# Kernel optimization log

Hardware: AMD Instinct MI355X
Metric: run time of the kernel (lower is better)

## Reference

```python
import jax, jax.numpy as jnp
import numpy as np

NUM_GRAPHS = 4096   # number of systems in the batch
NUM_ATOMS = 262144  # total ragged atoms (~64 per graph)
MODEL_DIMS = 512
VOCAB = 100         # atomic-number vocabulary


def setup_inputs() -> dict:
    key = jax.random.key(0)
    ks = jax.random.split(key, 8)
    atomic_numbers = jax.random.randint(ks[0], (NUM_ATOMS,), 0, VOCAB)
    pos = jax.random.normal(ks[1], (NUM_ATOMS, 3), dtype=jnp.float32)
    batch = jnp.sort(jax.random.randint(ks[2], (NUM_ATOMS,), 0, NUM_GRAPHS))
    embed = jax.random.normal(ks[3], (VOCAB, MODEL_DIMS), dtype=jnp.float32) * 0.02
    w_pos = jax.random.normal(ks[4], (3, MODEL_DIMS), dtype=jnp.float32) * 0.02
    w1 = jax.random.normal(ks[5], (MODEL_DIMS, MODEL_DIMS), dtype=jnp.float32) / np.sqrt(MODEL_DIMS)
    b1 = jnp.zeros((MODEL_DIMS,), dtype=jnp.float32)
    w2 = jax.random.normal(ks[6], (MODEL_DIMS, 1), dtype=jnp.float32) / np.sqrt(MODEL_DIMS)
    b2 = jnp.zeros((1,), dtype=jnp.float32)
    return dict(atomic_numbers=atomic_numbers, pos=pos, batch=batch,
                embed=embed, w_pos=w_pos, w1=w1, b1=b1, w2=w2, b2=b2)


def reference(atomic_numbers, pos, batch, embed, w_pos, w1, b1, w2, b2):
    # atom_rr.prepare_inputs: per-atom feature = type embedding + linear position
    # encoding, reduced to a per-graph mean (segment mean replaces the original
    # Python loop over ragged graph slices).
    feats = embed[atomic_numbers] + pos @ w_pos                      # [N, D]
    summed = jax.ops.segment_sum(feats, batch, num_segments=NUM_GRAPHS)    # [G, D]
    counts = jax.ops.segment_sum(jnp.ones((NUM_ATOMS,), feats.dtype), batch,
                                 num_segments=NUM_GRAPHS)            # [G]
    reduced = summed / jnp.maximum(counts, 1.0)[:, None]             # [G, D]
    # net: Linear -> GELU -> Linear
    h = jax.nn.gelu(reduced @ w1 + b1)                               # [G, D]
    energy = h @ w2 + b2                                             # [G, 1]
    return energy
```

## Files before the change

kernel.cpp:

```cpp
#include <hip/hip_runtime.h>
#include <hip/hip_bf16.h>
#include <math.h>

#define NATOMS 262144
#define NGRAPH 4096
#define DIM    512
#define VOC    100
#define GPB    16
#define KC     8
#define KLEN   (DIM / KC)
#define ROWS   104
#define HROW   104


__device__ __forceinline__ float gelu_tanh(float x) {
    const float c = 0.7978845608028654f;
    float x3 = x * x * x;
    return 0.5f * x * (1.0f + tanhf(c * (x + 0.044715f * x3)));
}

__device__ __forceinline__ int lower_bound(const int* __restrict__ a, int n, int t) {
    int lo = 0, hi = n;
    while (lo < hi) {
        int mid = (lo + hi) >> 1;
        if (a[mid] < t) lo = mid + 1; else hi = mid;
    }
    return lo;
}

__global__ void k_fused(const int* __restrict__ an, const float* __restrict__ pos,
                        const int* __restrict__ batch,
                        const float* __restrict__ embed, const float* __restrict__ w_pos,
                        const float* __restrict__ w1,
                        float* __restrict__ Hf, float* __restrict__ partial, int n) {
    const int t = threadIdx.x;

    if (blockIdx.x < NGRAPH / GPB) {
        const int g0 = blockIdx.x * GPB;

        __shared__ int   lh[GPB][VOC];
        __shared__ float lps[GPB][3];
        __shared__ int   lcnt[GPB];
        __shared__ int   range[2];

        for (int idx = t; idx < GPB * VOC; idx += 256) ((int*)lh)[idx] = 0;
        if (t < GPB * 3) ((float*)lps)[t] = 0.0f;
        if (t < GPB)     lcnt[t] = 0;
        if (t == 0) range[0] = lower_bound(batch, n, g0);
        if (t == 1) range[1] = lower_bound(batch, n, g0 + GPB);
        __syncthreads();

        const int lo = range[0], hi = range[1];

        for (int base = lo; base < hi; base += 256) {
            int i = base + t;
            bool act = (i < hi);
            int ic = act ? i : (hi - 1);
            int g = batch[ic];
            int rel = g - g0;

            float px = 0.f, py = 0.f, pz = 0.f;
            if (act) {
                int v = an[i];
                px = pos[3 * i + 0];
                py = pos[3 * i + 1];
                pz = pos[3 * i + 2];
                atomicAdd(&lh[rel][v], 1);
            }

            int lane = t & 63;
            int gFirst = __shfl(g, 0);
            int gLast  = __shfl(g, 63);
            if (gFirst == gLast) {
                float sx = px, sy = py, sz = pz;
                int   sc = act ? 1 : 0;
                #pragma unroll
                for (int off = 32; off; off >>= 1) {
                    sx += __shfl_down(sx, off);
                    sy += __shfl_down(sy, off);
                    sz += __shfl_down(sz, off);
                    sc += __shfl_down(sc, off);
                }
                if (lane == 0 && sc > 0) {
                    atomicAdd(&lps[rel][0], sx);
                    atomicAdd(&lps[rel][1], sy);
                    atomicAdd(&lps[rel][2], sz);
                    atomicAdd(&lcnt[rel], sc);
                }
            } else if (act) {
                atomicAdd(&lps[rel][0], px);
                atomicAdd(&lps[rel][1], py);
                atomicAdd(&lps[rel][2], pz);
                atomicAdd(&lcnt[rel], 1);
            }
        }
        __syncthreads();

        for (int idx = t; idx < GPB * HROW; idx += 256) {
            int u = idx / HROW, c = idx - u * HROW;
            float inv = 1.0f / fmaxf((float)lcnt[u], 1.0f);
            float val = 0.0f;
            if (c < VOC)          val = (float)lh[u][c] * inv;
            else if (c < VOC + 3) val = lps[u][c - VOC] * inv;
            Hf[(size_t)(g0 + u) * HROW + c] = val;
        }
    } else {
        const int mb = blockIdx.x - NGRAPH / GPB;
        const int kc = mb & (KC - 1);
        const int rc = mb >> 3;
        const int rt = rc >> 1;
        const int cc = rc & 1;
        const int j  = cc * 256 + t;
        const int r0 = rt * 8;
        const int k0 = kc * KLEN;

        __shared__ float s[8][KLEN];
        for (int idx = t; idx < 8 * KLEN; idx += 256) {
            int rr = idx / KLEN, k = idx & (KLEN - 1);
            int r = r0 + rr;
            float val = 0.0f;
            if (r < VOC)          val = embed[r * DIM + k0 + k];
            else if (r < VOC + 3) val = w_pos[(r - VOC) * DIM + k0 + k];
            s[rr][k] = val;
        }
        __syncthreads();

        float acc[8];
        #pragma unroll
        for (int rr = 0; rr < 8; rr++) acc[rr] = 0.0f;

        #pragma unroll 8
        for (int k = 0; k < KLEN; k++) {
            float w = w1[(k0 + k) * DIM + j];
            #pragma unroll
            for (int rr = 0; rr < 8; rr++)
                acc[rr] = fmaf(s[rr][k], w, acc[rr]);
        }

        #pragma unroll
        for (int rr = 0; rr < 8; rr++)
            partial[((size_t)kc * ROWS + r0 + rr) * DIM + j] = acc[rr];
    }
}

__global__ void k_reduce(const float* __restrict__ partial, float* __restrict__ M1) {
    int idx = blockIdx.x * 256 + threadIdx.x;
    if (idx >= 103 * DIM) return;
    int r = idx / DIM, j = idx - r * DIM;
    float sum = 0.0f;
    #pragma unroll
    for (int kc = 0; kc < KC; kc++)
        sum += partial[((size_t)kc * ROWS + r) * DIM + j];
    M1[r * DIM + j] = sum;
}

__global__ void k_final(const float* __restrict__ Hf, const float* __restrict__ M1,
                        const float* __restrict__ b1, const float* __restrict__ w2,
                        const float* __restrict__ b2, float* __restrict__ out) {
    const int G0 = blockIdx.x * 16;
    const int j = threadIdx.x;

    __shared__ float hT[HROW][20];
    __shared__ float part[8][16];

    for (int idx = j; idx < 16 * HROW; idx += 512) {
        int u = idx / HROW;
        int v = idx - u * HROW;
        hT[v][u] = Hf[(size_t)(G0 + u) * HROW + v];
    }
    __syncthreads();

    float acc[16];
    #pragma unroll
    for (int u = 0; u < 16; u++) acc[u] = 0.0f;

    for (int v = 0; v < VOC + 3; v++) {
        float m = M1[v * DIM + j];
        const float4* hp = (const float4*)(&hT[v][0]);
        float4 h0 = hp[0], h1 = hp[1], h2 = hp[2], h3 = hp[3];
        acc[ 0] = fmaf(h0.x, m, acc[ 0]);
        acc[ 1] = fmaf(h0.y, m, acc[ 1]);
        acc[ 2] = fmaf(h0.z, m, acc[ 2]);
        acc[ 3] = fmaf(h0.w, m, acc[ 3]);
        acc[ 4] = fmaf(h1.x, m, acc[ 4]);
        acc[ 5] = fmaf(h1.y, m, acc[ 5]);
        acc[ 6] = fmaf(h1.z, m, acc[ 6]);
        acc[ 7] = fmaf(h1.w, m, acc[ 7]);
        acc[ 8] = fmaf(h2.x, m, acc[ 8]);
        acc[ 9] = fmaf(h2.y, m, acc[ 9]);
        acc[10] = fmaf(h2.z, m, acc[10]);
        acc[11] = fmaf(h2.w, m, acc[11]);
        acc[12] = fmaf(h3.x, m, acc[12]);
        acc[13] = fmaf(h3.y, m, acc[13]);
        acc[14] = fmaf(h3.z, m, acc[14]);
        acc[15] = fmaf(h3.w, m, acc[15]);
    }

    float bj = b1[j];
    float wj = w2[j];
    float contrib[16];
    #pragma unroll
    for (int u = 0; u < 16; u++) {
        float pre = acc[u] + bj;
        contrib[u] = gelu_tanh(pre) * wj;
    }

    int wave = j >> 6;
    int lane = j & 63;
    #pragma unroll
    for (int u = 0; u < 16; u++) {
        float s = contrib[u];
        #pragma unroll
        for (int off = 32; off; off >>= 1) s += __shfl_down(s, off);
        if (lane == 0) part[wave][u] = s;
    }
    __syncthreads();

    if (j < 16) {
        float e = 0.0f;
        #pragma unroll
        for (int w = 0; w < 8; w++) e += part[w][j];
        out[G0 + j] = e + b2[0];
    }
}

extern "C" void kernel_launch(void* const* d_in, const int* in_sizes, int n_in,
                              void* d_out, int out_size, void* d_ws, size_t ws_size,
                              hipStream_t stream) {
    const int*   an    = (const int*)d_in[0];
    const float* pos   = (const float*)d_in[1];
    const int*   batch = (const int*)d_in[2];
    const float* embed = (const float*)d_in[3];
    const float* w_pos = (const float*)d_in[4];
    const float* w1    = (const float*)d_in[5];
    const float* b1    = (const float*)d_in[6];
    const float* w2    = (const float*)d_in[7];
    const float* b2    = (const float*)d_in[8];
    float* out = (float*)d_out;

    const int n = in_sizes[0];

    char* ws = (char*)d_ws;
    const size_t HF_B = (size_t)NGRAPH * HROW * 4;
    const size_t M1_B = (size_t)103 * DIM * 4;
    float* Hf      = (float*)ws;
    float* M1      = (float*)(ws + HF_B);
    float* partial = (float*)(ws + HF_B + M1_B);

    const int AB = NGRAPH / GPB;
    const int MB = 13 * 2 * KC;
    k_fused<<<AB + MB, 256, 0, stream>>>(an, pos, batch, embed, w_pos, w1,
                                         Hf, partial, n);
    k_reduce<<<(103 * DIM + 255) / 256, 256, 0, stream>>>(partial, M1);

    k_final<<<NGRAPH / 16, 512, 0, stream>>>(Hf, M1, b1, w2, b2, out);
}
```

Baseline: 111.5 us.

## Fuse three kernels into one cooperative kernel with grid-wide syncs

Merges the histogram/matmul, partial-reduce, and final GELU-projection kernels into a single cooperative launch of 512 blocks, separated by grid.sync() barriers. The final stage is re-tiled so each block handles 8 graphs with 256 threads covering two output columns each. The aim is to remove the launch gaps between kernels. In exchange it pays for two grid-wide barriers, and it falls back to the old three-kernel path if the cooperative launch fails.

New measurement: 231.0 us. 2.07x slower.

```diff
diff --git a/kernel.cpp b/kernel.cpp
--- a/kernel.cpp
+++ b/kernel.cpp
@@ -1,6 +1,8 @@
 #include <hip/hip_runtime.h>
-#include <hip/hip_bf16.h>
+#include <hip/hip_cooperative_groups.h>
 #include <math.h>
+
+namespace cg = cooperative_groups;
 
 #define NATOMS 262144
 #define NGRAPH 4096
@@ -11,6 +13,11 @@
 #define KLEN   (DIM / KC)
 #define ROWS   104
 #define HROW   104
+#define NBLK   512
+#define NTHR   256
+#define AB     256
+#define MB     208
+#define G3     8
 
 
 __device__ __forceinline__ float gelu_tanh(float x) {
@@ -28,22 +35,29 @@
     return lo;
 }
 
-__global__ void k_fused(const int* __restrict__ an, const float* __restrict__ pos,
-                        const int* __restrict__ batch,
-                        const float* __restrict__ embed, const float* __restrict__ w_pos,
-                        const float* __restrict__ w1,
-                        float* __restrict__ Hf, float* __restrict__ partial, int n) {
+__global__ void k_all(const int* __restrict__ an, const float* __restrict__ pos,
+                      const int* __restrict__ batch,
+                      const float* __restrict__ embed, const float* __restrict__ w_pos,
+                      const float* __restrict__ w1, const float* __restrict__ b1,
+                      const float* __restrict__ w2, const float* __restrict__ b2,
+                      float* __restrict__ Hf, float* __restrict__ partial,
+                      float* __restrict__ M1, float* __restrict__ out, int n) {
+    cg::grid_group grid = cg::this_grid();
+    const int b = blockIdx.x;
     const int t = threadIdx.x;
 
-    if (blockIdx.x < NGRAPH / GPB) {
-        const int g0 = blockIdx.x * GPB;
-
-        __shared__ int   lh[GPB][VOC];
-        __shared__ float lps[GPB][3];
-        __shared__ int   lcnt[GPB];
-        __shared__ int   range[2];
-
-        for (int idx = t; idx < GPB * VOC; idx += 256) ((int*)lh)[idx] = 0;
+    __shared__ int   lh[GPB][VOC];
+    __shared__ float lps[GPB][3];
+    __shared__ int   lcnt[GPB];
+    __shared__ int   range[2];
+    __shared__ float smat[8][KLEN];
+    __shared__ __align__(16) float hT[ROWS][G3];
+    __shared__ float part[4][G3];
+
+    if (b < AB) {
+        const int g0 = b * GPB;
+
+        for (int idx = t; idx < GPB * VOC; idx += NTHR) ((int*)lh)[idx] = 0;
         if (t < GPB * 3) ((float*)lps)[t] = 0.0f;
         if (t < GPB)     lcnt[t] = 0;
         if (t == 0) range[0] = lower_bound(batch, n, g0);
@@ -52,7 +66,7 @@
 
         const int lo = range[0], hi = range[1];
 
-        for (int base = lo; base < hi; base += 256) {
+        for (int base = lo; base < hi; base += NTHR) {
             int i = base + t;
             bool act = (i < hi);
             int ic = act ? i : (hi - 1);
@@ -96,6 +110,173 @@
         }
         __syncthreads();
 
+        for (int idx = t; idx < GPB * HROW; idx += NTHR) {
+            int u = idx / HROW, c = idx - u * HROW;
+            float inv = 1.0f / fmaxf((float)lcnt[u], 1.0f);
+            float val = 0.0f;
+            if (c < VOC)          val = (float)lh[u][c] * inv;
+            else if (c < VOC + 3) val = lps[u][c - VOC] * inv;
+            Hf[(size_t)(g0 + u) * HROW + c] = val;
+        }
+    } else if (b < AB + MB) {
+        const int mb = b - AB;
+        const int kc = mb & (KC - 1);
+        const int rc = mb >> 3;
+        const int rt = rc >> 1;
+        const int cc = rc & 1;
+        const int j  = cc * 256 + t;
+        const int r0 = rt * 8;
+        const int k0 = kc * KLEN;
+
+        for (int idx = t; idx < 8 * KLEN; idx += NTHR) {
+            int rr = idx / KLEN, k = idx & (KLEN - 1);
+            int r = r0 + rr;
+            float val = 0.0f;
+            if (r < VOC)          val = embed[r * DIM + k0 + k];
+            else if (r < VOC + 3) val = w_pos[(r - VOC) * DIM + k0 + k];
+            smat[rr][k] = val;
+        }
+        __syncthreads();
+
+        float acc[8];
+        #pragma unroll
+        for (int rr = 0; rr < 8; rr++) acc[rr] = 0.0f;
+
+        #pragma unroll 8
+        for (int k = 0; k < KLEN; k++) {
+            float w = w1[(k0 + k) * DIM + j];
+            #pragma unroll
+            for (int rr = 0; rr < 8; rr++)
+                acc[rr] = fmaf(smat[rr][k], w, acc[rr]);
+        }
+
+        #pragma unroll
+        for (int rr = 0; rr < 8; rr++)
+            partial[((size_t)kc * ROWS + r0 + rr) * DIM + j] = acc[rr];
+    }
+
+    grid.sync();
+
+    {
+        const int G0 = b * G3;
+        for (int idx = t; idx < G3 * HROW; idx += NTHR) {
+            int u = idx / HROW;
+            int v = idx - u * HROW;
+            hT[v][u] = Hf[(size_t)(G0 + u) * HROW + v];
+        }
+        int idx = b * NTHR + t;
+        if (idx < 103 * DIM) {
+            int r = idx / DIM, j = idx - r * DIM;
+            float sum = 0.0f;
+            #pragma unroll
+            for (int kc = 0; kc < KC; kc++)
+                sum += partial[((size_t)kc * ROWS + r) * DIM + j];
+            M1[r * DIM + j] = sum;
+        }
+    }
+
+    grid.sync();
+
+    {
+        const int G0 = b * G3;
+        float acc0[G3], acc1[G3];
+        #pragma unroll
+        for (int u = 0; u < G3; u++) { acc0[u] = 0.0f; acc1[u] = 0.0f; }
+
+        for (int v = 0; v < VOC + 3; v++) {
+            float m0 = M1[v * DIM + t];
+            float m1 = M1[v * DIM + t + 256];
+            const float4* hp = (const float4*)(&hT[v][0]);
+            float4 ha = hp[0], hb = hp[1];
+            acc0[0] = fmaf(ha.x, m0, acc0[0]);  acc1[0] = fmaf(ha.x, m1, acc1[0]);
+            acc0[1] = fmaf(ha.y, m0, acc0[1]);  acc1[1] = fmaf(ha.y, m1, acc1[1]);
+            acc0[2] = fmaf(ha.z, m0, acc0[2]);  acc1[2] = fmaf(ha.z, m1, acc1[2]);
+            acc0[3] = fmaf(ha.w, m0, acc0[3]);  acc1[3] = fmaf(ha.w, m1, acc1[3]);
+            acc0[4] = fmaf(hb.x, m0, acc0[4]);  acc1[4] = fmaf(hb.x, m1, acc1[4]);
+            acc0[5] = fmaf(hb.y, m0, acc0[5]);  acc1[5] = fmaf(hb.y, m1, acc1[5]);
+            acc0[6] = fmaf(hb.z, m0, acc0[6]);  acc1[6] = fmaf(hb.z, m1, acc1[6]);
+            acc0[7] = fmaf(hb.w, m0, acc0[7]);  acc1[7] = fmaf(hb.w, m1, acc1[7]);
+        }
+
+        float bj0 = b1[t],       bj1 = b1[t + 256];
+        float wj0 = w2[t],       wj1 = w2[t + 256];
+        float con[G3];
+        #pragma unroll
+        for (int u = 0; u < G3; u++)
+            con[u] = gelu_tanh(acc0[u] + bj0) * wj0 + gelu_tanh(acc1[u] + bj1) * wj1;
+
+        int wave = t >> 6;
+        int lane = t & 63;
+        #pragma unroll
+        for (int u = 0; u < G3; u++) {
+            float s = con[u];
+            #pragma unroll
+            for (int off = 32; off; off >>= 1) s += __shfl_down(s, off);
+            if (lane == 0) part[wave][u] = s;
+        }
+        __syncthreads();
+
+        if (t < G3)
+            out[G0 + t] = part[0][t] + part[1][t] + part[2][t] + part[3][t] + b2[0];
+    }
+}
+
+__global__ void k_fused(const int* __restrict__ an, const float* __restrict__ pos,
+                        const int* __restrict__ batch,
+                        const float* __restrict__ embed, const float* __restrict__ w_pos,
+                        const float* __restrict__ w1,
+                        float* __restrict__ Hf, float* __restrict__ partial, int n) {
+    const int t = threadIdx.x;
+
+    if (blockIdx.x < AB) {
+        const int g0 = blockIdx.x * GPB;
+        __shared__ int   lh[GPB][VOC];
+        __shared__ float lps[GPB][3];
+        __shared__ int   lcnt[GPB];
+        __shared__ int   range[2];
+
+        for (int idx = t; idx < GPB * VOC; idx += 256) ((int*)lh)[idx] = 0;
+        if (t < GPB * 3) ((float*)lps)[t] = 0.0f;
+        if (t < GPB)     lcnt[t] = 0;
+        if (t == 0) range[0] = lower_bound(batch, n, g0);
+        if (t == 1) range[1] = lower_bound(batch, n, g0 + GPB);
+        __syncthreads();
+
+        const int lo = range[0], hi = range[1];
+        for (int base = lo; base < hi; base += 256) {
+            int i = base + t;
+            bool act = (i < hi);
+            int ic = act ? i : (hi - 1);
+            int g = batch[ic];
+            int rel = g - g0;
+            float px = 0.f, py = 0.f, pz = 0.f;
+            if (act) {
+                int v = an[i];
+                px = pos[3 * i]; py = pos[3 * i + 1]; pz = pos[3 * i + 2];
+                atomicAdd(&lh[rel][v], 1);
+            }
+            int lane = t & 63;
+            int gFirst = __shfl(g, 0);
+            int gLast  = __shfl(g, 63);
+            if (gFirst == gLast) {
+                float sx = px, sy = py, sz = pz;
+                int sc = act ? 1 : 0;
+                #pragma unroll
+                for (int off = 32; off; off >>= 1) {
+                    sx += __shfl_down(sx, off); sy += __shfl_down(sy, off);
+                    sz += __shfl_down(sz, off); sc += __shfl_down(sc, off);
+                }
+                if (lane == 0 && sc > 0) {
+                    atomicAdd(&lps[rel][0], sx); atomicAdd(&lps[rel][1], sy);
+                    atomicAdd(&lps[rel][2], sz); atomicAdd(&lcnt[rel], sc);
+                }
+            } else if (act) {
+                atomicAdd(&lps[rel][0], px); atomicAdd(&lps[rel][1], py);
+                atomicAdd(&lps[rel][2], pz); atomicAdd(&lcnt[rel], 1);
+            }
+        }
+        __syncthreads();
+
         for (int idx = t; idx < GPB * HROW; idx += 256) {
             int u = idx / HROW, c = idx - u * HROW;
             float inv = 1.0f / fmaxf((float)lcnt[u], 1.0f);
@@ -105,7 +286,7 @@
             Hf[(size_t)(g0 + u) * HROW + c] = val;
         }
     } else {
-        const int mb = blockIdx.x - NGRAPH / GPB;
+        const int mb = blockIdx.x - AB;
         const int kc = mb & (KC - 1);
         const int rc = mb >> 3;
         const int rt = rc >> 1;
@@ -128,7 +309,6 @@
         float acc[8];
         #pragma unroll
         for (int rr = 0; rr < 8; rr++) acc[rr] = 0.0f;
-
         #pragma unroll 8
         for (int k = 0; k < KLEN; k++) {
             float w = w1[(k0 + k) * DIM + j];
@@ -136,7 +316,6 @@
             for (int rr = 0; rr < 8; rr++)
                 acc[rr] = fmaf(s[rr][k], w, acc[rr]);
         }
-
         #pragma unroll
         for (int rr = 0; rr < 8; rr++)
             partial[((size_t)kc * ROWS + r0 + rr) * DIM + j] = acc[rr];
@@ -160,7 +339,7 @@
     const int G0 = blockIdx.x * 16;
     const int j = threadIdx.x;
 
-    __shared__ float hT[HROW][20];
+    __shared__ __align__(16) float hT[HROW][20];
     __shared__ float part[8][16];
 
     for (int idx = j; idx < 16 * HROW; idx += 512) {
@@ -178,32 +357,22 @@
         float m = M1[v * DIM + j];
         const float4* hp = (const float4*)(&hT[v][0]);
         float4 h0 = hp[0], h1 = hp[1], h2 = hp[2], h3 = hp[3];
-        acc[ 0] = fmaf(h0.x, m, acc[ 0]);
-        acc[ 1] = fmaf(h0.y, m, acc[ 1]);
-        acc[ 2] = fmaf(h0.z, m, acc[ 2]);
-        acc[ 3] = fmaf(h0.w, m, acc[ 3]);
-        acc[ 4] = fmaf(h1.x, m, acc[ 4]);
-        acc[ 5] = fmaf(h1.y, m, acc[ 5]);
-        acc[ 6] = fmaf(h1.z, m, acc[ 6]);
-        acc[ 7] = fmaf(h1.w, m, acc[ 7]);
-        acc[ 8] = fmaf(h2.x, m, acc[ 8]);
-        acc[ 9] = fmaf(h2.y, m, acc[ 9]);
-        acc[10] = fmaf(h2.z, m, acc[10]);
-        acc[11] = fmaf(h2.w, m, acc[11]);
-        acc[12] = fmaf(h3.x, m, acc[12]);
-        acc[13] = fmaf(h3.y, m, acc[13]);
-        acc[14] = fmaf(h3.z, m, acc[14]);
-        acc[15] = fmaf(h3.w, m, acc[15]);
+        acc[ 0] = fmaf(h0.x, m, acc[ 0]); acc[ 1] = fmaf(h0.y, m, acc[ 1]);
+        acc[ 2] = fmaf(h0.z, m, acc[ 2]); acc[ 3] = fmaf(h0.w, m, acc[ 3]);
+        acc[ 4] = fmaf(h1.x, m, acc[ 4]); acc[ 5] = fmaf(h1.y, m, acc[ 5]);
+        acc[ 6] = fmaf(h1.z, m, acc[ 6]); acc[ 7] = fmaf(h1.w, m, acc[ 7]);
+        acc[ 8] = fmaf(h2.x, m, acc[ 8]); acc[ 9] = fmaf(h2.y, m, acc[ 9]);
+        acc[10] = fmaf(h2.z, m, acc[10]); acc[11] = fmaf(h2.w, m, acc[11]);
+        acc[12] = fmaf(h3.x, m, acc[12]); acc[13] = fmaf(h3.y, m, acc[13]);
+        acc[14] = fmaf(h3.z, m, acc[14]); acc[15] = fmaf(h3.w, m, acc[15]);
     }
 
     float bj = b1[j];
     float wj = w2[j];
     float contrib[16];
     #pragma unroll
-    for (int u = 0; u < 16; u++) {
-        float pre = acc[u] + bj;
-        contrib[u] = gelu_tanh(pre) * wj;
-    }
+    for (int u = 0; u < 16; u++)
+        contrib[u] = gelu_tanh(acc[u] + bj) * wj;
 
     int wave = j >> 6;
     int lane = j & 63;
@@ -238,7 +407,7 @@
     const float* b2    = (const float*)d_in[8];
     float* out = (float*)d_out;
 
-    const int n = in_sizes[0];
+    int n = in_sizes[0];
 
     char* ws = (char*)d_ws;
     const size_t HF_B = (size_t)NGRAPH * HROW * 4;
@@ -247,11 +416,15 @@
     float* M1      = (float*)(ws + HF_B);
     float* partial = (float*)(ws + HF_B + M1_B);
 
-    const int AB = NGRAPH / GPB;
-    const int MB = 13 * 2 * KC;
-    k_fused<<<AB + MB, 256, 0, stream>>>(an, pos, batch, embed, w_pos, w1,
-                                         Hf, partial, n);
-    k_reduce<<<(103 * DIM + 255) / 256, 256, 0, stream>>>(partial, M1);
-
-    k_final<<<NGRAPH / 16, 512, 0, stream>>>(Hf, M1, b1, w2, b2, out);
-}
+    void* args[] = {(void*)&an, (void*)&pos, (void*)&batch, (void*)&embed,
+                    (void*)&w_pos, (void*)&w1, (void*)&b1, (void*)&w2, (void*)&b2,
+                    (void*)&Hf, (void*)&partial, (void*)&M1, (void*)&out, (void*)&n};
+    hipError_t err = hipLaunchCooperativeKernel((const void*)k_all, dim3(NBLK),
+                                                dim3(NTHR), args, 0, stream);
+    if (err != hipSuccess) {
+        k_fused<<<AB + MB, 256, 0, stream>>>(an, pos, batch, embed, w_pos, w1,
+                                             Hf, partial, n);
+        k_reduce<<<(103 * DIM + 255) / 256, 256, 0, stream>>>(partial, M1);
+        k_final<<<NGRAPH / 16, 512, 0, stream>>>(Hf, M1, b1, w2, b2, out);
+    }
+}
```

## Fold split-K reduction into fused kernel via in-block LDS reduction

Applied to the files above, without the earlier changes.

The embed×W1 precompute blocks now cover all of K inside one block: eight 32-thread slices each take 64 k-values, and the block sums their partials through a shared-memory reduction before writing M1 directly. This removes the separate k_reduce launch and the partial-sum round trip through global memory. Shared memory is a union so the histogram and matrix paths share it, and hT gets explicit 16-byte alignment. The cost is a larger per-block shared tile (8×512 floats), more matmul blocks (208) with narrower 32-column slices, and two extra barriers.

New measurement: 120.7 us. +8.3%, slower.

```diff
diff --git a/kernel.cpp b/kernel.cpp
--- a/kernel.cpp
+++ b/kernel.cpp
@@ -1,5 +1,4 @@
 #include <hip/hip_runtime.h>
-#include <hip/hip_bf16.h>
 #include <math.h>
 
 #define NATOMS 262144
@@ -7,10 +6,9 @@
 #define DIM    512
 #define VOC    100
 #define GPB    16
-#define KC     8
-#define KLEN   (DIM / KC)
-#define ROWS   104
 #define HROW   104
+#define AB     256
+#define MBLK   208
 
 
 __device__ __forceinline__ float gelu_tanh(float x) {
@@ -28,29 +26,35 @@
     return lo;
 }
 
+struct AccumS {
+    int   lh[GPB][VOC];
+    float lps[GPB][3];
+    int   lcnt[GPB];
+    int   range[2];
+};
+struct MatS {
+    float smat[8][DIM];
+};
+
 __global__ void k_fused(const int* __restrict__ an, const float* __restrict__ pos,
                         const int* __restrict__ batch,
                         const float* __restrict__ embed, const float* __restrict__ w_pos,
                         const float* __restrict__ w1,
-                        float* __restrict__ Hf, float* __restrict__ partial, int n) {
+                        float* __restrict__ Hf, float* __restrict__ M1, int n) {
     const int t = threadIdx.x;
-
-    if (blockIdx.x < NGRAPH / GPB) {
+    __shared__ union { AccumS a; MatS m; } sm;
+
+    if (blockIdx.x < AB) {
         const int g0 = blockIdx.x * GPB;
 
-        __shared__ int   lh[GPB][VOC];
-        __shared__ float lps[GPB][3];
-        __shared__ int   lcnt[GPB];
-        __shared__ int   range[2];
-
-        for (int idx = t; idx < GPB * VOC; idx += 256) ((int*)lh)[idx] = 0;
-        if (t < GPB * 3) ((float*)lps)[t] = 0.0f;
-        if (t < GPB)     lcnt[t] = 0;
-        if (t == 0) range[0] = lower_bound(batch, n, g0);
-        if (t == 1) range[1] = lower_bound(batch, n, g0 + GPB);
-        __syncthreads();
-
-        const int lo = range[0], hi = range[1];
+        for (int idx = t; idx < GPB * VOC; idx += 256) ((int*)sm.a.lh)[idx] = 0;
+        if (t < GPB * 3) ((float*)sm.a.lps)[t] = 0.0f;
+        if (t < GPB)     sm.a.lcnt[t] = 0;
+        if (t == 0) sm.a.range[0] = lower_bound(batch, n, g0);
+        if (t == 1) sm.a.range[1] = lower_bound(batch, n, g0 + GPB);
+        __syncthreads();
+
+        const int lo = sm.a.range[0], hi = sm.a.range[1];
 
         for (int base = lo; base < hi; base += 256) {
             int i = base + t;
@@ -65,7 +69,7 @@
                 px = pos[3 * i + 0];
                 py = pos[3 * i + 1];
                 pz = pos[3 * i + 2];
-                atomicAdd(&lh[rel][v], 1);
+                atomicAdd(&sm.a.lh[rel][v], 1);
             }
 
             int lane = t & 63;
@@ -82,46 +86,46 @@
                     sc += __shfl_down(sc, off);
                 }
                 if (lane == 0 && sc > 0) {
-                    atomicAdd(&lps[rel][0], sx);
-                    atomicAdd(&lps[rel][1], sy);
-                    atomicAdd(&lps[rel][2], sz);
-                    atomicAdd(&lcnt[rel], sc);
+                    atomicAdd(&sm.a.lps[rel][0], sx);
+                    atomicAdd(&sm.a.lps[rel][1], sy);
+                    atomicAdd(&sm.a.lps[rel][2], sz);
+                    atomicAdd(&sm.a.lcnt[rel], sc);
                 }
             } else if (act) {
-                atomicAdd(&lps[rel][0], px);
-                atomicAdd(&lps[rel][1], py);
-                atomicAdd(&lps[rel][2], pz);
-                atomicAdd(&lcnt[rel], 1);
+                atomicAdd(&sm.a.lps[rel][0], px);
+                atomicAdd(&sm.a.lps[rel][1], py);
+                atomicAdd(&sm.a.lps[rel][2], pz);
+                atomicAdd(&sm.a.lcnt[rel], 1);
             }
         }
         __syncthreads();
 
         for (int idx = t; idx < GPB * HROW; idx += 256) {
             int u = idx / HROW, c = idx - u * HROW;
-            float inv = 1.0f / fmaxf((float)lcnt[u], 1.0f);
+            float inv = 1.0f / fmaxf((float)sm.a.lcnt[u], 1.0f);
             float val = 0.0f;
-            if (c < VOC)          val = (float)lh[u][c] * inv;
-            else if (c < VOC + 3) val = lps[u][c - VOC] * inv;
+            if (c < VOC)          val = (float)sm.a.lh[u][c] * inv;
+            else if (c < VOC + 3) val = sm.a.lps[u][c - VOC] * inv;
             Hf[(size_t)(g0 + u) * HROW + c] = val;
         }
     } else {
-        const int mb = blockIdx.x - NGRAPH / GPB;
-        const int kc = mb & (KC - 1);
-        const int rc = mb >> 3;
-        const int rt = rc >> 1;
-        const int cc = rc & 1;
-        const int j  = cc * 256 + t;
+        const int mb = blockIdx.x - AB;
+        const int rt = mb / 16;
+        const int cc = mb - rt * 16;
         const int r0 = rt * 8;
-        const int k0 = kc * KLEN;
-
-        __shared__ float s[8][KLEN];
-        for (int idx = t; idx < 8 * KLEN; idx += 256) {
-            int rr = idx / KLEN, k = idx & (KLEN - 1);
-            int r = r0 + rr;
+        const int c  = t & 31;
+        const int s  = t >> 5;
+        const int j  = cc * 32 + c;
+        const int k0 = s * 64;
+
+        for (int idx = t; idx < 8 * DIM; idx += 256) {
+            int rr = idx >> 9;
+            int k  = idx & (DIM - 1);
+            int r  = r0 + rr;
             float val = 0.0f;
-            if (r < VOC)          val = embed[r * DIM + k0 + k];
-            else if (r < VOC + 3) val = w_pos[(r - VOC) * DIM + k0 + k];
-            s[rr][k] = val;
+            if (r < VOC)          val = embed[r * DIM + k];
+            else if (r < VOC + 3) val = w_pos[(r - VOC) * DIM + k];
+            sm.m.smat[rr][k] = val;
         }
         __syncthreads();
 
@@ -130,28 +134,31 @@
         for (int rr = 0; rr < 8; rr++) acc[rr] = 0.0f;
 
         #pragma unroll 8
-        for (int k = 0; k < KLEN; k++) {
+        for (int k = 0; k < 64; k++) {
             float w = w1[(k0 + k) * DIM + j];
             #pragma unroll
             for (int rr = 0; rr < 8; rr++)
-                acc[rr] = fmaf(s[rr][k], w, acc[rr]);
-        }
-
+                acc[rr] = fmaf(sm.m.smat[rr][k0 + k], w, acc[rr]);
+        }
+        __syncthreads();
+
+        float* red = &sm.m.smat[0][0];
         #pragma unroll
         for (int rr = 0; rr < 8; rr++)
-            partial[((size_t)kc * ROWS + r0 + rr) * DIM + j] = acc[rr];
-    }
-}
-
-__global__ void k_reduce(const float* __restrict__ partial, float* __restrict__ M1) {
-    int idx = blockIdx.x * 256 + threadIdx.x;
-    if (idx >= 103 * DIM) return;
-    int r = idx / DIM, j = idx - r * DIM;
-    float sum = 0.0f;
-    #pragma unroll
-    for (int kc = 0; kc < KC; kc++)
-        sum += partial[((size_t)kc * ROWS + r) * DIM + j];
-    M1[r * DIM + j] = sum;
+            red[(s * 8 + rr) * 32 + c] = acc[rr];
+        __syncthreads();
+
+        {
+            int r = t >> 5;
+            float sum = 0.0f;
+            #pragma unroll
+            for (int ss = 0; ss < 8; ss++)
+                sum += red[(ss * 8 + r) * 32 + (t & 31)];
+            int row = r0 + r;
+            if (row < VOC + 3)
+                M1[row * DIM + cc * 32 + (t & 31)] = sum;
+        }
+    }
 }
 
 __global__ void k_final(const float* __restrict__ Hf, const float* __restrict__ M1,
@@ -160,7 +167,7 @@
     const int G0 = blockIdx.x * 16;
     const int j = threadIdx.x;
 
-    __shared__ float hT[HROW][20];
+    __shared__ __align__(16) float hT[HROW][20];
     __shared__ float part[8][16];
 
     for (int idx = j; idx < 16 * HROW; idx += 512) {
@@ -178,32 +185,22 @@
         float m = M1[v * DIM + j];
         const float4* hp = (const float4*)(&hT[v][0]);
         float4 h0 = hp[0], h1 = hp[1], h2 = hp[2], h3 = hp[3];
-        acc[ 0] = fmaf(h0.x, m, acc[ 0]);
-        acc[ 1] = fmaf(h0.y, m, acc[ 1]);
-        acc[ 2] = fmaf(h0.z, m, acc[ 2]);
-        acc[ 3] = fmaf(h0.w, m, acc[ 3]);
-        acc[ 4] = fmaf(h1.x, m, acc[ 4]);
-        acc[ 5] = fmaf(h1.y, m, acc[ 5]);
-        acc[ 6] = fmaf(h1.z, m, acc[ 6]);
-        acc[ 7] = fmaf(h1.w, m, acc[ 7]);
-        acc[ 8] = fmaf(h2.x, m, acc[ 8]);
-        acc[ 9] = fmaf(h2.y, m, acc[ 9]);
-        acc[10] = fmaf(h2.z, m, acc[10]);
-        acc[11] = fmaf(h2.w, m, acc[11]);
-        acc[12] = fmaf(h3.x, m, acc[12]);
-        acc[13] = fmaf(h3.y, m, acc[13]);
-        acc[14] = fmaf(h3.z, m, acc[14]);
-        acc[15] = fmaf(h3.w, m, acc[15]);
+        acc[ 0] = fmaf(h0.x, m, acc[ 0]); acc[ 1] = fmaf(h0.y, m, acc[ 1]);
+        acc[ 2] = fmaf(h0.z, m, acc[ 2]); acc[ 3] = fmaf(h0.w, m, acc[ 3]);
+        acc[ 4] = fmaf(h1.x, m, acc[ 4]); acc[ 5] = fmaf(h1.y, m, acc[ 5]);
+        acc[ 6] = fmaf(h1.z, m, acc[ 6]); acc[ 7] = fmaf(h1.w, m, acc[ 7]);
+        acc[ 8] = fmaf(h2.x, m, acc[ 8]); acc[ 9] = fmaf(h2.y, m, acc[ 9]);
+        acc[10] = fmaf(h2.z, m, acc[10]); acc[11] = fmaf(h2.w, m, acc[11]);
+        acc[12] = fmaf(h3.x, m, acc[12]); acc[13] = fmaf(h3.y, m, acc[13]);
+        acc[14] = fmaf(h3.z, m, acc[14]); acc[15] = fmaf(h3.w, m, acc[15]);
     }
 
     float bj = b1[j];
     float wj = w2[j];
     float contrib[16];
     #pragma unroll
-    for (int u = 0; u < 16; u++) {
-        float pre = acc[u] + bj;
-        contrib[u] = gelu_tanh(pre) * wj;
-    }
+    for (int u = 0; u < 16; u++)
+        contrib[u] = gelu_tanh(acc[u] + bj) * wj;
 
     int wave = j >> 6;
     int lane = j & 63;
@@ -242,16 +239,11 @@
 
     char* ws = (char*)d_ws;
     const size_t HF_B = (size_t)NGRAPH * HROW * 4;
-    const size_t M1_B = (size_t)103 * DIM * 4;
-    float* Hf      = (float*)ws;
-    float* M1      = (float*)(ws + HF_B);
-    float* partial = (float*)(ws + HF_B + M1_B);
-
-    const int AB = NGRAPH / GPB;
-    const int MB = 13 * 2 * KC;
-    k_fused<<<AB + MB, 256, 0, stream>>>(an, pos, batch, embed, w_pos, w1,
-                                         Hf, partial, n);
-    k_reduce<<<(103 * DIM + 255) / 256, 256, 0, stream>>>(partial, M1);
+    float* Hf = (float*)ws;
+    float* M1 = (float*)(ws + HF_B);
+
+    k_fused<<<AB + MBLK, 256, 0, stream>>>(an, pos, batch, embed, w_pos, w1,
+                                           Hf, M1, n);
 
     k_final<<<NGRAPH / 16, 512, 0, stream>>>(Hf, M1, b1, w2, b2, out);
 }
```
